# Kernel optimization log

Hardware: AMD Instinct MI355X
Metric: run time of the kernel (lower is better)

Reference implementation:

```python
import jax, jax.numpy as jnp
import numpy as np

HIDDEN = 768
N_HEADS = 12
HEAD_DIM = HIDDEN // N_HEADS  # 64 (multihead=True)
NEG_BIG = -1e31


def setup_inputs() -> dict:
    key = jax.random.key(0)
    ks = jax.random.split(key, 8)
    B, S = 4, 2048
    toks = jax.random.normal(ks[0], (B, S, HIDDEN), dtype=jnp.float32)
    masks = jax.random.randint(ks[1], (B, S), 0, 2, dtype=jnp.int32)
    s = 0.02
    Wq = jax.random.normal(ks[2], (HIDDEN, HIDDEN), dtype=jnp.float32) * s
    Wk = jax.random.normal(ks[3], (HIDDEN, HIDDEN), dtype=jnp.float32) * s
    Wv = jax.random.normal(ks[4], (HIDDEN, HIDDEN), dtype=jnp.float32) * s
    bq = jax.random.normal(ks[5], (HIDDEN,), dtype=jnp.float32) * s
    bk = jax.random.normal(ks[6], (HIDDEN,), dtype=jnp.float32) * s
    bv = jax.random.normal(ks[7], (HIDDEN,), dtype=jnp.float32) * s
    return {"toks": toks, "masks": masks, "Wq": Wq, "bq": bq,
            "Wk": Wk, "bk": bk, "Wv": Wv, "bv": bv}


def reference(toks, masks, Wq, bq, Wk, bk, Wv, bv):
    B, S, D = toks.shape
    m = masks.astype(jnp.float32)  # [B,S]
    # additive outer-product padding mask: (1 - m_i*m_j) * -1e31, shape [B,S,S]
    add_mask = (1.0 - m[:, :, None] * m[:, None, :]) * NEG_BIG

    def split_heads(x):  # [B,S,D] -> [B,H,S,hd]
        return x.reshape(B, S, N_HEADS, HEAD_DIM).transpose(0, 2, 1, 3)

    q = split_heads(toks @ Wq + bq)
    k = split_heads(toks @ Wk + bk)
    v = split_heads(toks @ Wv + bv)

    scores = jnp.einsum("bhqd,bhkd->bhqk", q, k) / jnp.sqrt(
        jnp.asarray(HEAD_DIM, dtype=toks.dtype))
    scores = scores + add_mask[:, None, :, :]
    probs = jax.nn.softmax(scores, axis=-1)  # dropout is identity at eval
    ctx = jnp.einsum("bhqk,bhkd->bhqd", probs, v)
    return ctx.transpose(0, 2, 1, 3).reshape(B, S, D)
```

## Files before the change

kernel.cpp:

```cpp
#include <hip/hip_runtime.h>
#include <hip/hip_bf16.h>
#include <cstddef>


typedef __bf16 bf16_8 __attribute__((ext_vector_type(8)));
typedef float f32x4 __attribute__((ext_vector_type(4)));
typedef short s16x4 __attribute__((ext_vector_type(4)));
typedef short s16x8 __attribute__((ext_vector_type(8)));

#define HID 768
#define NHEADS 12
#define HD 64
#define BATCH 4
#define SEQ 2048
#define NEGBIG2 (-1.44269504e31f)
#define SCALE2 0.18033688f

#define KT 32
#define NKT (SEQ / KT)
#define STR 68
#define VSTR 36
#define ASTR 40

static __device__ __forceinline__ f32x4 mfma16x16x32(bf16_8 a, bf16_8 b, f32x4 c) {
  return __builtin_amdgcn_mfma_f32_16x16x32_bf16(a, b, c, 0, 0, 0);
}

static __device__ __forceinline__ void lds_barrier() {
  __asm__ volatile("s_waitcnt lgkmcnt(0)\n\ts_barrier" ::: "memory");
}

static __device__ __forceinline__ void lds_flush() {
  __asm__ volatile("s_waitcnt lgkmcnt(0)" ::: "memory");
}

static __device__ __forceinline__ float fast_exp2(float x) {
#if __has_builtin(__builtin_amdgcn_exp2f)
  return __builtin_amdgcn_exp2f(x);
#else
  return __expf(x * 0.69314718f);
#endif
}

static __device__ __forceinline__ s16x4 pack_bf16x4(f32x4 p) {
  s16x4 o;
#pragma unroll
  for (int i = 0; i < 4; ++i) {
    __bf16 b = (__bf16)p[i];
    o[i] = __builtin_bit_cast(short, b);
  }
  return o;
}

static __device__ __forceinline__ bf16_8 cat2(const __bf16* p) {
  s16x4 lo = *(const s16x4*)p;
  s16x4 hi = *(const s16x4*)(p + 4);
  s16x8 v = __builtin_shufflevector(lo, hi, 0, 1, 2, 3, 4, 5, 6, 7);
  return __builtin_bit_cast(bf16_8, v);
}

static __device__ __forceinline__ void write2(__bf16* p, s16x8 v) {
  *(s16x4*)p = __builtin_shufflevector(v, v, 0, 1, 2, 3);
  *(s16x4*)(p + 4) = __builtin_shufflevector(v, v, 4, 5, 6, 7);
}

static __device__ __forceinline__ bf16_8 cvt_a_frag(const float* p) {
  f32x4 af0 = *(const f32x4*)p;
  f32x4 af1 = *(const f32x4*)(p + 4);
  bf16_8 a;
  a[0] = (__bf16)af0[0]; a[1] = (__bf16)af0[1];
  a[2] = (__bf16)af0[2]; a[3] = (__bf16)af0[3];
  a[4] = (__bf16)af1[0]; a[5] = (__bf16)af1[1];
  a[6] = (__bf16)af1[2]; a[7] = (__bf16)af1[3];
  return a;
}

__global__ __launch_bounds__(256) void mask_kadd(const int* __restrict__ masks,
                                                 float* __restrict__ kaddG) {
  int i = blockIdx.x * 256 + threadIdx.x;
  kaddG[i] = masks[i] ? 0.0f : NEGBIG2;
}

__global__ __launch_bounds__(256) void transpose768x3(const float* __restrict__ Wq,
                                                      const float* __restrict__ Wk,
                                                      const float* __restrict__ Wv,
                                                      __bf16* __restrict__ WtBase) {
  const float* in = blockIdx.z == 0 ? Wq : (blockIdx.z == 1 ? Wk : Wv);
  __bf16* out = WtBase + (size_t)blockIdx.z * HID * HID;
  __shared__ __bf16 tile[32][33];
  int bx = blockIdx.x * 32, by = blockIdx.y * 32;
  int tx = threadIdx.x, ty = threadIdx.y;
#pragma unroll
  for (int r = 0; r < 32; r += 8)
    tile[ty + r][tx] = (__bf16)in[(size_t)(by + ty + r) * HID + bx + tx];
  __syncthreads();
#pragma unroll
  for (int r = 0; r < 32; r += 8)
    out[(size_t)(bx + ty + r) * HID + by + tx] = tile[tx][ty + r];
}

__global__ __launch_bounds__(256, 4) void proj_kv(const float* __restrict__ toks,
                                                  const __bf16* __restrict__ WtK,
                                                  const float* __restrict__ bk,
                                                  const __bf16* __restrict__ WtV,
                                                  const float* __restrict__ bv,
                                                  __bf16* __restrict__ Kout,
                                                  __bf16* __restrict__ Vtout,
                                                  int head0, int hm) {
  __shared__ __align__(16) __bf16 ldsA[2][64 * ASTR];
  int tid = threadIdx.x;
  int w = tid >> 6, lane = tid & 63, l16 = lane & 15, quad = lane >> 4;
  int m0 = blockIdx.x * 64;
  int hl = blockIdx.y, h = head0 + hl;
  int srow = tid >> 2, scg = tid & 3;
  const float* asrc = toks + (size_t)(m0 + srow) * HID + scg * 8;
  const __bf16* bKrow = WtK + (size_t)(h * 64 + w * 16 + l16) * HID + quad * 8;
  const __bf16* bVrow = WtV + (size_t)(h * 64 + w * 16 + l16) * HID + quad * 8;
  f32x4 zero = {0.f, 0.f, 0.f, 0.f};
  f32x4 aK[4], aV[4];
#pragma unroll
  for (int mt = 0; mt < 4; ++mt) { aK[mt] = zero; aV[mt] = zero; }

  *(bf16_8*)(&ldsA[0][srow * ASTR + scg * 8]) = cvt_a_frag(asrc);
  __syncthreads();

  const int NCH = HID / 32;
  for (int t = 0; t < NCH; ++t) {
    int b = t & 1;
    int kk = t * 32;
    bf16_8 areg;
    if (t + 1 < NCH) areg = cvt_a_frag(asrc + kk + 32);
    bf16_8 bkf = *(const bf16_8*)(bKrow + kk);
    bf16_8 bvf = *(const bf16_8*)(bVrow + kk);
#pragma unroll
    for (int mt = 0; mt < 4; ++mt) {
      bf16_8 af = *(const bf16_8*)(&ldsA[b][(mt * 16 + l16) * ASTR + quad * 8]);
      aK[mt] = mfma16x16x32(af, bkf, aK[mt]);
      aV[mt] = mfma16x16x32(af, bvf, aV[mt]);
    }
    if (t + 1 < NCH) {
      *(bf16_8*)(&ldsA[b ^ 1][srow * ASTR + scg * 8]) = areg;
      lds_barrier();
    }
  }

  int d = w * 16 + l16;
  float bnK = bk[h * 64 + d];
  float bnV = bv[h * 64 + d];
#pragma unroll
  for (int mt = 0; mt < 4; ++mt) {
#pragma unroll
    for (int r = 0; r < 4; ++r) {
      int m = m0 + mt * 16 + quad * 4 + r;
      int b = m >> 11;
      int s = m & (SEQ - 1);
      Kout[(((size_t)b * hm + hl) * SEQ + s) * HD + d] = (__bf16)(aK[mt][r] + bnK);
      Vtout[(((size_t)b * hm + hl) * HD + d) * SEQ + s] = (__bf16)(aV[mt][r] + bnV);
    }
  }
}

__global__ __launch_bounds__(256, 6) void attn_fused(const float* __restrict__ toks,
                                                     const __bf16* __restrict__ WtQ,
                                                     const float* __restrict__ bq,
                                                     const __bf16* __restrict__ Kbuf,
                                                     const __bf16* __restrict__ Vtbuf,
                                                     const float* __restrict__ kaddG,
                                                     float* __restrict__ out,
                                                     int head0, int hm) {
  __shared__ __align__(16) __bf16 ldsK[2][KT * STR];
  __shared__ __align__(16) __bf16 ldsV[2][64 * VSTR];
  __shared__ __align__(16) __bf16 ldsQP[64 * STR];
  int tid = threadIdx.x;
  int w = tid >> 6, lane = tid & 63, l16 = lane & 15, quad = lane >> 4;

  int nwg = gridDim.x * gridDim.y * gridDim.z;
  int hwf = blockIdx.x + gridDim.x * (blockIdx.y + gridDim.y * blockIdx.z);
  int lg = (hwf & 7) * (nwg >> 3) + (hwf >> 3);
  int q0 = (lg & (gridDim.x - 1)) * 64;
  int grp = lg / gridDim.x;
  int hl = grp % hm, bz = grp / hm;
  int h = head0 + hl;

  const float* kb = kaddG + (size_t)bz * SEQ;
  f32x4 zero = {0.f, 0.f, 0.f, 0.f};

  const __bf16* Kb = Kbuf + ((size_t)bz * hm + hl) * SEQ * HD;
  const __bf16* Vb = Vtbuf + ((size_t)bz * hm + hl) * HD * SEQ;
  __bf16* Pw = &ldsQP[(w * 16) * STR];

  {
    const float* arow = toks + ((size_t)bz * SEQ + q0 + w * 16 + l16) * HID + quad * 8;
    const __bf16* brow = WtQ + (size_t)(h * 64 + l16) * HID + quad * 8;
    f32x4 qa[4] = {zero, zero, zero, zero};
    for (int kk = 0; kk < HID; kk += 32) {
      bf16_8 a = cvt_a_frag(arow + kk);
#pragma unroll
      for (int t = 0; t < 4; ++t)
        qa[t] = mfma16x16x32(a, *(const bf16_8*)(brow + (size_t)t * 16 * HID + kk), qa[t]);
    }
#pragma unroll
    for (int t = 0; t < 4; ++t) {
      float bn = bq[h * 64 + t * 16 + l16];
#pragma unroll
      for (int r = 0; r < 4; ++r)
        Pw[(quad * 4 + r) * STR + t * 16 + l16] = (__bf16)(qa[t][r] + bn);
    }
  }
  lds_flush();

  bf16_8 qf[2];
#pragma unroll
  for (int half = 0; half < 2; ++half)
    qf[half] = cat2(&Pw[l16 * STR + half * 32 + quad * 8]);
  float actq = (kb[q0 + w * 16 + l16] == 0.0f) ? 1.0f : 0.0f;

  int srow = tid >> 3, sc = tid & 7;
  int vrow = tid >> 2, vc = tid & 3;
  {
    s16x8 k0 = *(const s16x8*)(Kb + (size_t)srow * HD + sc * 8);
    s16x8 v0 = *(const s16x8*)(Vb + (size_t)vrow * SEQ + vc * 8);
    write2(&ldsK[0][srow * STR + sc * 8], k0);
    write2(&ldsV[0][vrow * VSTR + vc * 8], v0);
  }
  s16x8 kA = *(const s16x8*)(Kb + (size_t)(KT + srow) * HD + sc * 8);
  s16x8 vA = *(const s16x8*)(Vb + (size_t)vrow * SEQ + KT + vc * 8);
  s16x8 kB, vB;
  lds_barrier();

  float lsum = 0.f;
  f32x4 acc[4];
#pragma unroll
  for (int dt = 0; dt < 4; ++dt) acc[dt] = zero;

  auto body = [&](int buf, int t) __attribute__((always_inline)) {
    int j0 = t * KT;
#pragma unroll
    for (int kbk = 0; kbk < 2; ++kbk) {
      bf16_8 kf0 = cat2(&ldsK[buf][(kbk * 16 + l16) * STR + quad * 8]);
      bf16_8 kf1 = cat2(&ldsK[buf][(kbk * 16 + l16) * STR + 32 + quad * 8]);
      f32x4 st = mfma16x16x32(kf1, qf[1], mfma16x16x32(kf0, qf[0], zero));
      f32x4 ck = *(const f32x4*)(kb + j0 + kbk * 16 + quad * 4);
      f32x4 p;
#pragma unroll
      for (int r = 0; r < 4; ++r) {
        float v = actq * fmaf(st[r], SCALE2, ck[r]);
        p[r] = fast_exp2(v);
      }
      lsum += p[0] + p[1] + p[2] + p[3];
      *(s16x4*)(&Pw[l16 * STR + kbk * 16 + quad * 4]) = pack_bf16x4(p);
    }
    lds_flush();
    bf16_8 pf = cat2(&Pw[l16 * STR + quad * 8]);
#pragma unroll
    for (int dt = 0; dt < 4; ++dt) {
      bf16_8 vf = cat2(&ldsV[buf][(dt * 16 + l16) * VSTR + quad * 8]);
      acc[dt] = mfma16x16x32(pf, vf, acc[dt]);
    }
  };

  for (int t = 0; t < NKT; t += 2) {
    {
      int j2 = (t + 2 < NKT) ? (t + 2) * KT : 0;
      kB = *(const s16x8*)(Kb + (size_t)(j2 + srow) * HD + sc * 8);
      vB = *(const s16x8*)(Vb + (size_t)vrow * SEQ + j2 + vc * 8);
    }
    body(0, t);
    write2(&ldsK[1][srow * STR + sc * 8], kA);
    write2(&ldsV[1][vrow * VSTR + vc * 8], vA);
    lds_barrier();
    {
      int j3 = (t + 3 < NKT) ? (t + 3) * KT : 0;
      kA = *(const s16x8*)(Kb + (size_t)(j3 + srow) * HD + sc * 8);
      vA = *(const s16x8*)(Vb + (size_t)vrow * SEQ + j3 + vc * 8);
    }
    body(1, t + 1);
    write2(&ldsK[0][srow * STR + sc * 8], kB);
    write2(&ldsV[0][vrow * VSTR + vc * 8], vB);
    lds_barrier();
  }

  float v = lsum;
  v += __shfl_xor(v, 16);
  v += __shfl_xor(v, 32);
  float linv = 1.0f / v;
  float lr[4];
#pragma unroll
  for (int r = 0; r < 4; ++r) lr[r] = __shfl(linv, quad * 4 + r);
#pragma unroll
  for (int dt = 0; dt < 4; ++dt)
#pragma unroll
    for (int r = 0; r < 4; ++r)
      out[((size_t)bz * SEQ + q0 + w * 16 + quad * 4 + r) * HID + h * HD + dt * 16 + l16] =
          acc[dt][r] * lr[r];
}

extern "C" void kernel_launch(void* const* d_in, const int* in_sizes, int n_in,
                              void* d_out, int out_size, void* d_ws, size_t ws_size,
                              hipStream_t stream) {
  (void)in_sizes; (void)n_in; (void)out_size;
  const float* toks = (const float*)d_in[0];
  const int* masks = (const int*)d_in[1];
  const float* Wq = (const float*)d_in[2];
  const float* bq = (const float*)d_in[3];
  const float* Wk = (const float*)d_in[4];
  const float* bk = (const float*)d_in[5];
  const float* Wv = (const float*)d_in[6];
  const float* bv = (const float*)d_in[7];
  char* ws = (char*)d_ws;
  const size_t KADD_B = (size_t)BATCH * SEQ * 4;
  const size_t WT_B = (size_t)HID * HID * 2;
  const size_t KV_FULL_B = (size_t)BATCH * NHEADS * SEQ * HD * 2;
  const size_t KV_HEAD_B = (size_t)BATCH * SEQ * HD * 2;
  const size_t TIER_A_NEED = KADD_B + 3 * WT_B + 2 * KV_FULL_B;
  float* kaddG = (float*)(ws);
  __bf16* WtQ = (__bf16*)(ws + KADD_B + 0 * WT_B);
  __bf16* WtK = (__bf16*)(ws + KADD_B + 1 * WT_B);
  __bf16* WtV = (__bf16*)(ws + KADD_B + 2 * WT_B);
  float* outp = (float*)d_out;

  mask_kadd<<<BATCH * SEQ / 256, 256, 0, stream>>>(masks, kaddG);
  dim3 tgrid(HID / 32, HID / 32, 3), tblk(32, 8);
  transpose768x3<<<tgrid, tblk, 0, stream>>>(Wq, Wk, Wv, WtQ);

  if (ws_size >= TIER_A_NEED) {
    __bf16* Kf = (__bf16*)(ws + KADD_B + 3 * WT_B);
    __bf16* Vtf = (__bf16*)(ws + KADD_B + 3 * WT_B + KV_FULL_B);
    dim3 pgrid(BATCH * SEQ / 64, NHEADS);
    proj_kv<<<pgrid, 256, 0, stream>>>(toks, WtK, bk, WtV, bv, Kf, Vtf, 0, NHEADS);
    dim3 agrid(SEQ / 64, NHEADS, BATCH);
    attn_fused<<<agrid, 256, 0, stream>>>(toks, WtQ, bq, Kf, Vtf, kaddG, outp, 0, NHEADS);
  } else {
    __bf16* Kh = (__bf16*)(ws + KADD_B + 3 * WT_B);
    __bf16* Vth = (__bf16*)(ws + KADD_B + 3 * WT_B + KV_HEAD_B);
    dim3 pgrid(BATCH * SEQ / 64, 1);
    dim3 agrid(SEQ / 64, 1, BATCH);
    for (int h = 0; h < NHEADS; ++h) {
      proj_kv<<<pgrid, 256, 0, stream>>>(toks, WtK, bk, WtV, bv, Kh, Vth, h, 1);
      attn_fused<<<agrid, 256, 0, stream>>>(toks, WtQ, bq, Kh, Vth, kaddG, outp, h, 1);
    }
  }
}
```

Baseline: 327.0 us.

## Load K/V fragments directly from global memory and pass P via shuffles

Removes the LDS staging of K and V tiles and the block barriers. Each wave now loads its MFMA fragments straight from global memory, relying on cache for the reuse across the four waves, and prefetches the next K tile. The P matrix is moved into the A-operand layout with lane shuffles instead of an LDS round trip. Occupancy hint lowered to 4. This trades barrier and LDS traffic for redundant global/L2 loads per wave and extra shuffle work.

Result: slower. 594.9 us (+81.9%).

```diff
diff --git a/kernel.cpp b/kernel.cpp
--- a/kernel.cpp
+++ b/kernel.cpp
@@ -7,6 +7,7 @@
 typedef float f32x4 __attribute__((ext_vector_type(4)));
 typedef short s16x4 __attribute__((ext_vector_type(4)));
 typedef short s16x8 __attribute__((ext_vector_type(8)));
+typedef unsigned int u32x4 __attribute__((ext_vector_type(4)));
 
 #define HID 768
 #define NHEADS 12
@@ -19,7 +20,6 @@
 #define KT 32
 #define NKT (SEQ / KT)
 #define STR 68
-#define VSTR 36
 #define ASTR 40
 
 static __device__ __forceinline__ f32x4 mfma16x16x32(bf16_8 a, bf16_8 b, f32x4 c) {
@@ -42,14 +42,10 @@
 #endif
 }
 
-static __device__ __forceinline__ s16x4 pack_bf16x4(f32x4 p) {
-  s16x4 o;
-#pragma unroll
-  for (int i = 0; i < 4; ++i) {
-    __bf16 b = (__bf16)p[i];
-    o[i] = __builtin_bit_cast(short, b);
-  }
-  return o;
+static __device__ __forceinline__ unsigned pkbf(float a, float b) {
+  unsigned lo = (unsigned)__builtin_bit_cast(unsigned short, (__bf16)a);
+  unsigned hi = (unsigned)__builtin_bit_cast(unsigned short, (__bf16)b);
+  return lo | (hi << 16);
 }
 
 static __device__ __forceinline__ bf16_8 cat2(const __bf16* p) {
@@ -57,11 +53,6 @@
   s16x4 hi = *(const s16x4*)(p + 4);
   s16x8 v = __builtin_shufflevector(lo, hi, 0, 1, 2, 3, 4, 5, 6, 7);
   return __builtin_bit_cast(bf16_8, v);
-}
-
-static __device__ __forceinline__ void write2(__bf16* p, s16x8 v) {
-  *(s16x4*)p = __builtin_shufflevector(v, v, 0, 1, 2, 3);
-  *(s16x4*)(p + 4) = __builtin_shufflevector(v, v, 4, 5, 6, 7);
 }
 
 static __device__ __forceinline__ bf16_8 cvt_a_frag(const float* p) {
@@ -160,7 +151,7 @@
   }
 }
 
-__global__ __launch_bounds__(256, 6) void attn_fused(const float* __restrict__ toks,
+__global__ __launch_bounds__(256, 4) void attn_fused(const float* __restrict__ toks,
                                                      const __bf16* __restrict__ WtQ,
                                                      const float* __restrict__ bq,
                                                      const __bf16* __restrict__ Kbuf,
@@ -168,9 +159,7 @@
                                                      const float* __restrict__ kaddG,
                                                      float* __restrict__ out,
                                                      int head0, int hm) {
-  __shared__ __align__(16) __bf16 ldsK[2][KT * STR];
-  __shared__ __align__(16) __bf16 ldsV[2][64 * VSTR];
-  __shared__ __align__(16) __bf16 ldsQP[64 * STR];
+  __shared__ __align__(16) __bf16 ldsQ[64 * STR];
   int tid = threadIdx.x;
   int w = tid >> 6, lane = tid & 63, l16 = lane & 15, quad = lane >> 4;
 
@@ -187,7 +176,7 @@
 
   const __bf16* Kb = Kbuf + ((size_t)bz * hm + hl) * SEQ * HD;
   const __bf16* Vb = Vtbuf + ((size_t)bz * hm + hl) * HD * SEQ;
-  __bf16* Pw = &ldsQP[(w * 16) * STR];
+  __bf16* Qw = &ldsQ[(w * 16) * STR];
 
   {
     const float* arow = toks + ((size_t)bz * SEQ + q0 + w * 16 + l16) * HID + quad * 8;
@@ -204,80 +193,84 @@
       float bn = bq[h * 64 + t * 16 + l16];
 #pragma unroll
       for (int r = 0; r < 4; ++r)
-        Pw[(quad * 4 + r) * STR + t * 16 + l16] = (__bf16)(qa[t][r] + bn);
+        Qw[(quad * 4 + r) * STR + t * 16 + l16] = (__bf16)(qa[t][r] + bn);
     }
   }
   lds_flush();
 
-  bf16_8 qf[2];
-#pragma unroll
-  for (int half = 0; half < 2; ++half)
-    qf[half] = cat2(&Pw[l16 * STR + half * 32 + quad * 8]);
+  bf16_8 qf0 = cat2(&Qw[l16 * STR + quad * 8]);
+  bf16_8 qf1 = cat2(&Qw[l16 * STR + 32 + quad * 8]);
   float actq = (kb[q0 + w * 16 + l16] == 0.0f) ? 1.0f : 0.0f;
 
-  int srow = tid >> 3, sc = tid & 7;
-  int vrow = tid >> 2, vc = tid & 3;
-  {
-    s16x8 k0 = *(const s16x8*)(Kb + (size_t)srow * HD + sc * 8);
-    s16x8 v0 = *(const s16x8*)(Vb + (size_t)vrow * SEQ + vc * 8);
-    write2(&ldsK[0][srow * STR + sc * 8], k0);
-    write2(&ldsV[0][vrow * VSTR + vc * 8], v0);
-  }
-  s16x8 kA = *(const s16x8*)(Kb + (size_t)(KT + srow) * HD + sc * 8);
-  s16x8 vA = *(const s16x8*)(Vb + (size_t)vrow * SEQ + KT + vc * 8);
-  s16x8 kB, vB;
-  lds_barrier();
+  const __bf16* kR00 = Kb + (size_t)l16 * HD + quad * 8;
+  const __bf16* kR01 = kR00 + 32;
+  const __bf16* kR10 = kR00 + (size_t)16 * HD;
+  const __bf16* kR11 = kR10 + 32;
+  const __bf16* vR0 = Vb + (size_t)l16 * SEQ + quad * 8;
+  const __bf16* vR1 = vR0 + (size_t)16 * SEQ;
+  const __bf16* vR2 = vR0 + (size_t)32 * SEQ;
+  const __bf16* vR3 = vR0 + (size_t)48 * SEQ;
+  const float* ckB = kb + quad * 4;
+
+  s16x8 kc00 = *(const s16x8*)(kR00);
+  s16x8 kc01 = *(const s16x8*)(kR01);
+  s16x8 kc10 = *(const s16x8*)(kR10);
+  s16x8 kc11 = *(const s16x8*)(kR11);
 
   float lsum = 0.f;
-  f32x4 acc[4];
-#pragma unroll
-  for (int dt = 0; dt < 4; ++dt) acc[dt] = zero;
-
-  auto body = [&](int buf, int t) __attribute__((always_inline)) {
+  f32x4 acc0 = zero, acc1 = zero, acc2 = zero, acc3 = zero;
+  bool hiq = (quad & 2) != 0;
+  int src0 = l16 + ((quad & 1) << 5);
+  int src1 = src0 + 16;
+
+  for (int t = 0; t < NKT; ++t) {
     int j0 = t * KT;
-#pragma unroll
-    for (int kbk = 0; kbk < 2; ++kbk) {
-      bf16_8 kf0 = cat2(&ldsK[buf][(kbk * 16 + l16) * STR + quad * 8]);
-      bf16_8 kf1 = cat2(&ldsK[buf][(kbk * 16 + l16) * STR + 32 + quad * 8]);
-      f32x4 st = mfma16x16x32(kf1, qf[1], mfma16x16x32(kf0, qf[0], zero));
-      f32x4 ck = *(const f32x4*)(kb + j0 + kbk * 16 + quad * 4);
-      f32x4 p;
-#pragma unroll
-      for (int r = 0; r < 4; ++r) {
-        float v = actq * fmaf(st[r], SCALE2, ck[r]);
-        p[r] = fast_exp2(v);
-      }
-      lsum += p[0] + p[1] + p[2] + p[3];
-      *(s16x4*)(&Pw[l16 * STR + kbk * 16 + quad * 4]) = pack_bf16x4(p);
-    }
-    lds_flush();
-    bf16_8 pf = cat2(&Pw[l16 * STR + quad * 8]);
-#pragma unroll
-    for (int dt = 0; dt < 4; ++dt) {
-      bf16_8 vf = cat2(&ldsV[buf][(dt * 16 + l16) * VSTR + quad * 8]);
-      acc[dt] = mfma16x16x32(pf, vf, acc[dt]);
-    }
-  };
-
-  for (int t = 0; t < NKT; t += 2) {
-    {
-      int j2 = (t + 2 < NKT) ? (t + 2) * KT : 0;
-      kB = *(const s16x8*)(Kb + (size_t)(j2 + srow) * HD + sc * 8);
-      vB = *(const s16x8*)(Vb + (size_t)vrow * SEQ + j2 + vc * 8);
-    }
-    body(0, t);
-    write2(&ldsK[1][srow * STR + sc * 8], kA);
-    write2(&ldsV[1][vrow * VSTR + vc * 8], vA);
-    lds_barrier();
-    {
-      int j3 = (t + 3 < NKT) ? (t + 3) * KT : 0;
-      kA = *(const s16x8*)(Kb + (size_t)(j3 + srow) * HD + sc * 8);
-      vA = *(const s16x8*)(Vb + (size_t)vrow * SEQ + j3 + vc * 8);
-    }
-    body(1, t + 1);
-    write2(&ldsK[0][srow * STR + sc * 8], kB);
-    write2(&ldsV[0][vrow * VSTR + vc * 8], vB);
-    lds_barrier();
+    int jn = (t + 1 < NKT) ? j0 + KT : 0;
+    f32x4 ck0 = *(const f32x4*)(ckB + j0);
+    f32x4 ck1 = *(const f32x4*)(ckB + j0 + 16);
+    s16x8 vf0 = *(const s16x8*)(vR0 + j0);
+    s16x8 vf1 = *(const s16x8*)(vR1 + j0);
+    s16x8 vf2 = *(const s16x8*)(vR2 + j0);
+    s16x8 vf3 = *(const s16x8*)(vR3 + j0);
+    s16x8 kn00 = *(const s16x8*)(kR00 + (size_t)jn * HD);
+    s16x8 kn01 = *(const s16x8*)(kR01 + (size_t)jn * HD);
+    s16x8 kn10 = *(const s16x8*)(kR10 + (size_t)jn * HD);
+    s16x8 kn11 = *(const s16x8*)(kR11 + (size_t)jn * HD);
+
+    f32x4 st0 = mfma16x16x32(__builtin_bit_cast(bf16_8, kc01), qf1,
+                             mfma16x16x32(__builtin_bit_cast(bf16_8, kc00), qf0, zero));
+    f32x4 st1 = mfma16x16x32(__builtin_bit_cast(bf16_8, kc11), qf1,
+                             mfma16x16x32(__builtin_bit_cast(bf16_8, kc10), qf0, zero));
+    f32x4 p0, p1;
+#pragma unroll
+    for (int r = 0; r < 4; ++r) {
+      p0[r] = fast_exp2(actq * fmaf(st0[r], SCALE2, ck0[r]));
+      p1[r] = fast_exp2(actq * fmaf(st1[r], SCALE2, ck1[r]));
+    }
+    lsum += p0[0] + p0[1] + p0[2] + p0[3] + p1[0] + p1[1] + p1[2] + p1[3];
+    unsigned s0 = pkbf(p0[0], p0[1]);
+    unsigned s1 = pkbf(p0[2], p0[3]);
+    unsigned s2 = pkbf(p1[0], p1[1]);
+    unsigned s3 = pkbf(p1[2], p1[3]);
+    unsigned a00 = (unsigned)__shfl((int)s0, src0);
+    unsigned a02 = (unsigned)__shfl((int)s2, src0);
+    unsigned a10 = (unsigned)__shfl((int)s1, src0);
+    unsigned a12 = (unsigned)__shfl((int)s3, src0);
+    unsigned a20 = (unsigned)__shfl((int)s0, src1);
+    unsigned a22 = (unsigned)__shfl((int)s2, src1);
+    unsigned a30 = (unsigned)__shfl((int)s1, src1);
+    unsigned a32 = (unsigned)__shfl((int)s3, src1);
+    u32x4 pd;
+    pd[0] = hiq ? a02 : a00;
+    pd[1] = hiq ? a12 : a10;
+    pd[2] = hiq ? a22 : a20;
+    pd[3] = hiq ? a32 : a30;
+    bf16_8 pa = __builtin_bit_cast(bf16_8, pd);
+    acc0 = mfma16x16x32(pa, __builtin_bit_cast(bf16_8, vf0), acc0);
+    acc1 = mfma16x16x32(pa, __builtin_bit_cast(bf16_8, vf1), acc1);
+    acc2 = mfma16x16x32(pa, __builtin_bit_cast(bf16_8, vf2), acc2);
+    acc3 = mfma16x16x32(pa, __builtin_bit_cast(bf16_8, vf3), acc3);
+    kc00 = kn00; kc01 = kn01; kc10 = kn10; kc11 = kn11;
   }
 
   float v = lsum;
@@ -287,12 +280,13 @@
   float lr[4];
 #pragma unroll
   for (int r = 0; r < 4; ++r) lr[r] = __shfl(linv, quad * 4 + r);
+  f32x4 accs[4] = {acc0, acc1, acc2, acc3};
 #pragma unroll
   for (int dt = 0; dt < 4; ++dt)
 #pragma unroll
     for (int r = 0; r < 4; ++r)
       out[((size_t)bz * SEQ + q0 + w * 16 + quad * 4 + r) * HID + h * HD + dt * 16 + l16] =
-          acc[dt][r] * lr[r];
+          accs[dt][r] * lr[r];
 }
 
 extern "C" void kernel_launch(void* const* d_in, const int* in_sizes, int n_in,
```
